# Kernel optimization log

Measured on AMD Instinct MI355X. Metric: run time of the kernel, lower is better.

The kernel has to match this reference:

```python
import jax, jax.numpy as jnp
import numpy as np

B, MAX_NPUS, MEM_SIZE = 16, 1024, 4096
IN_SIZE, REG_SIZE, MEM_DIM = 512, 256, 128
GRU_IN = IN_SIZE + MEM_DIM
MMU_OUT = MEM_DIM * 5 + 4  # 644


def setup_inputs() -> dict:
    key = jax.random.key(0)
    ks = jax.random.split(key, 12)
    s = 0.02
    return {
        "input_vector": jax.random.normal(ks[0], (B, IN_SIZE), jnp.float32),
        "registers": jax.random.normal(ks[1], (B, MAX_NPUS, REG_SIZE), jnp.float32),
        "memory_context": jax.random.normal(ks[2], (B, MEM_SIZE, MEM_DIM), jnp.float32),
        "W_ih": jax.random.normal(ks[3], (3 * REG_SIZE, GRU_IN), jnp.float32) * s,
        "b_ih": jax.random.normal(ks[4], (3 * REG_SIZE,), jnp.float32) * s,
        "W_hh": jax.random.normal(ks[5], (3 * REG_SIZE, REG_SIZE), jnp.float32) * s,
        "b_hh": jax.random.normal(ks[6], (3 * REG_SIZE,), jnp.float32) * s,
        "W_mmu": jax.random.normal(ks[7], (MMU_OUT, REG_SIZE), jnp.float32) * s,
        "b_mmu": jax.random.normal(ks[8], (MMU_OUT,), jnp.float32) * s,
        "W_out": jax.random.normal(ks[9], (IN_SIZE, REG_SIZE), jnp.float32) * s,
        "b_out": jax.random.normal(ks[10], (IN_SIZE,), jnp.float32) * s,
        "active_npus": MAX_NPUS,
    }


def reference(input_vector, registers, memory_context, W_ih, b_ih, W_hh, b_hh,
              W_mmu, b_mmu, W_out, b_out, active_npus):
    md, rs = MEM_DIM, REG_SIZE
    curr = registers[:, :active_npus, :]                      # [B,N,rs]
    mmu = jnp.einsum('bnr,or->bno', curr, W_mmu) + b_mmu      # [B,N,5*md+4]
    query = mmu[..., :md]
    w_key = mmu[..., md:2 * md]
    w_val = mmu[..., 2 * md:3 * md]
    w_gate = jax.nn.sigmoid(mmu[..., 3 * md:3 * md + 1])
    ssd_key = mmu[..., 3 * md + 1:4 * md + 1]
    ssd_val = mmu[..., 4 * md + 1:5 * md + 1]
    ssd_gate = jax.nn.softmax(mmu[..., 5 * md + 1:5 * md + 4], axis=-1)
    # attention read over shared memory
    scores = jnp.einsum('bnd,bmd->bnm', query, memory_context) / jnp.sqrt(jnp.float32(md))
    attn = jax.nn.softmax(scores, axis=-1)                    # [B,N,M]
    read_data = jnp.einsum('bnm,bmd->bnd', attn, memory_context)
    # GRU cell (torch GRUCell semantics, gate order r,z,n)
    inp = jnp.broadcast_to(input_vector[:, None, :], (curr.shape[0], active_npus, input_vector.shape[-1]))
    x = jnp.concatenate([inp, read_data], axis=-1)            # [B,N,in+md]
    gi = jnp.einsum('bni,oi->bno', x, W_ih) + b_ih            # [B,N,3*rs]
    gh = jnp.einsum('bnr,or->bno', curr, W_hh) + b_hh
    gi_r, gi_z, gi_n = gi[..., :rs], gi[..., rs:2 * rs], gi[..., 2 * rs:]
    gh_r, gh_z, gh_n = gh[..., :rs], gh[..., rs:2 * rs], gh[..., 2 * rs:]
    r = jax.nn.sigmoid(gi_r + gh_r)
    z = jax.nn.sigmoid(gi_z + gh_z)
    n = jnp.tanh(gi_n + r * gh_n)
    new_regs = (1.0 - z) * n + z * curr                       # [B,N,rs]
    output_active = jnp.einsum('bnr,or->bno', new_regs, W_out) + b_out
    return (output_active, new_regs, w_key, w_val, w_gate, ssd_key, ssd_val, ssd_gate)
```

## Files before the change

kernel.cpp:

```cpp
#include <hip/hip_runtime.h>
#include <hip/hip_bf16.h>
#include <math.h>

#define B_      16
#define NPUS    1024
#define MEMS    4096
#define INS     512
#define RS      256
#define MD      128
#define GRUIN   640
#define MMUO    644
#define NROWS   (B_*NPUS)

#define O_OUT   0u
#define O_REGS  8388608u
#define O_WKEY  12582912u
#define O_WVAL  14680064u
#define O_WGATE 16777216u
#define O_SSDK  16793600u
#define O_SSDV  18890752u
#define O_SSDG  20987904u

typedef __attribute__((ext_vector_type(8))) short bf16x8;
typedef __attribute__((ext_vector_type(4))) float f32x4;
typedef __attribute__((ext_vector_type(4))) unsigned short u16x4;

__device__ __forceinline__ float sigf(float x){ return 1.f/(1.f+__expf(-x)); }
__device__ __forceinline__ unsigned short bfu(float x){
    __hip_bfloat16 h = __float2bfloat16(x);
    return __builtin_bit_cast(unsigned short, h);
}
__device__ __forceinline__ float b2f(unsigned short u){
    unsigned v = ((unsigned)u) << 16;
    return __builtin_bit_cast(float, v);
}
__device__ __forceinline__ void gload16(const void* g, void* s)
{
    __builtin_amdgcn_global_load_lds(
        (const __attribute__((address_space(1))) void*)g,
        (__attribute__((address_space(3))) void*)s, 16, 0, 0);
}

__global__ __launch_bounds__(256) void k_cvt(const float* __restrict__ src,
                                             unsigned short* __restrict__ dst, int n4)
{
    int i = blockIdx.x*256 + threadIdx.x;
    if (i >= n4) return;
    float4 v = ((const float4*)src)[i];
    u16x4 o = { bfu(v.x), bfu(v.y), bfu(v.z), bfu(v.w) };
    ((u16x4*)dst)[i] = o;
}

__global__ __launch_bounds__(256) void k_cvt5(const float* __restrict__ s0, unsigned short* __restrict__ d0,
                                              const float* __restrict__ s1, unsigned short* __restrict__ d1,
                                              const float* __restrict__ s2, unsigned short* __restrict__ d2,
                                              const float* __restrict__ s3, unsigned short* __restrict__ d3,
                                              const float* __restrict__ s4, unsigned short* __restrict__ d4)
{
    int gi = blockIdx.x*256 + threadIdx.x;
    const float* s; unsigned short* d; int idx;
    if      (gi < 41216)  { s = s0; d = d0; idx = gi; }
    else if (gi < 164096) { s = s1; d = d1; idx = gi - 41216; }
    else if (gi < 213248) { s = s2; d = d2; idx = gi - 164096; }
    else if (gi < 246016) { s = s3; d = d3; idx = gi - 213248; }
    else                  { s = s4; d = d4; idx = gi - 246016; }
    float4 v = ((const float4*)s)[idx];
    u16x4 o = { bfu(v.x), bfu(v.y), bfu(v.z), bfu(v.w) };
    ((u16x4*)d)[idx] = o;
}

__global__ __launch_bounds__(256) void k_gi(const float* __restrict__ inp,
                                            const float* __restrict__ Wih,
                                            float* __restrict__ gi0)
{
    __shared__ float xs[INS];
    const int b = blockIdx.x, seg = blockIdx.y;
    const int t = threadIdx.x;
    for (int i = t; i < INS; i += 256) xs[i] = inp[(size_t)b*INS + i];
    __syncthreads();
    const int o = seg*256 + t;
    const float* wrow = Wih + (size_t)o*GRUIN;
    float a0 = 0.f, a1 = 0.f, a2 = 0.f, a3 = 0.f;
    for (int k = 0; k < INS; k += 4) {
        float4 wv = *(const float4*)(wrow + k);
        a0 += xs[k]*wv.x; a1 += xs[k+1]*wv.y; a2 += xs[k+2]*wv.z; a3 += xs[k+3]*wv.w;
    }
    gi0[(size_t)b*768 + o] = (a0 + a1) + (a2 + a3);
}

__global__ __launch_bounds__(256) void k_conv(const float* __restrict__ mem,
                                              __hip_bfloat16* __restrict__ memB,
                                              __hip_bfloat16* __restrict__ memT)
{
    __shared__ float Ms[32][129];
    const int t = threadIdx.x;
    const int b = blockIdx.x >> 7;
    const int m0 = (blockIdx.x & 127) << 5;
    const float* src = mem + ((size_t)b*MEMS + m0)*MD;
    for (int idx = t; idx < 32*128; idx += 256) {
        int m = idx >> 7, d = idx & 127;
        float v = src[(size_t)m*MD + d];
        Ms[m][d] = v;
        memB[((size_t)b*MEMS + m0 + m)*MD + d] = __float2bfloat16(v);
    }
    __syncthreads();
    for (int idx = t; idx < 128*32; idx += 256) {
        int d = idx >> 5, m = idx & 31;
        memT[((size_t)b*MD + d)*MEMS + m0 + m] = __float2bfloat16(Ms[m][d]);
    }
}

__global__ __launch_bounds__(256, 4) void k_mmu(const __hip_bfloat16* __restrict__ Ab,
                                                const __hip_bfloat16* __restrict__ Wb,
                                                const float* __restrict__ bias,
                                                float* __restrict__ out,
                                                __hip_bfloat16* __restrict__ qbf)
{
    __shared__ __hip_bfloat16 At[2][64][32];
    __shared__ __hip_bfloat16 Bt[2][128][32];
    const int t = threadIdx.x, w = t >> 6, l = t & 63;
    const int lg = l >> 4, ll = l & 15;
    const int m0 = blockIdx.x*64;
    const int n0 = blockIdx.y*128;
    f32x4 acc[8];
    #pragma unroll
    for (int c = 0; c < 8; c++) acc[c] = (f32x4){0,0,0,0};

    const char* aSrc;
    {
        int row = t >> 2, cc = t & 3;
        int gc = cc ^ ((row >> 1) & 3);
        aSrc = (const char*)((const short*)Ab + (size_t)(m0+row)*RS) + gc*16;
    }
    const char* bSrc[2];
    #pragma unroll
    for (int j = 0; j < 2; j++) {
        int ci = w*128 + j*64 + l;
        int row = ci >> 2, cc = ci & 3;
        int gc = cc ^ ((row >> 1) & 3);
        bSrc[j] = (const char*)((const short*)Wb + (size_t)(n0+row)*RS) + gc*16;
    }

    auto stage = [&](int buf, int it) {
        int off = it*64;
        char* abase = (char*)(&At[buf][0][0]) + (size_t)(w << 6)*16;
        gload16(aSrc + off, abase);
        #pragma unroll
        for (int j = 0; j < 2; j++) {
            char* bbase = (char*)(&Bt[buf][0][0]) + (size_t)(w*128 + j*64)*16;
            gload16(bSrc[j] + off, bbase);
        }
    };

    stage(0, 0);
    asm volatile("s_waitcnt vmcnt(0)" ::: "memory");
    __syncthreads();
    int cur = 0;
    const int arow = (w << 4) + ll;
    const int aswz = ((lg ^ ((arow >> 1) & 3)) << 4);
    for (int it = 0; it < 8; ++it) {
        if (it + 1 < 8) stage(cur ^ 1, it + 1);
        const char* ab = (const char*)(&At[cur][0][0]);
        const char* bb = (const char*)(&Bt[cur][0][0]);
        bf16x8 af = *(const bf16x8*)(ab + arow*64 + aswz);
        #pragma unroll
        for (int c = 0; c < 8; c++) {
            int r0 = c*16 + ll;
            int sw = ((lg ^ ((r0 >> 1) & 3)) << 4);
            bf16x8 bf = *(const bf16x8*)(bb + (size_t)r0*64 + sw);
            acc[c] = __builtin_amdgcn_mfma_f32_16x16x32_bf16(af, bf, acc[c], 0, 0, 0);
        }
        asm volatile("s_waitcnt vmcnt(0)" ::: "memory");
        __syncthreads();
        cur ^= 1;
    }
    const int wm0 = m0 + (w << 4);
    #pragma unroll
    for (int c = 0; c < 8; c++) {
        int o = n0 + c*16 + ll;
        if (o > 640) continue;
        float bv = bias[o];
        #pragma unroll
        for (int r = 0; r < 4; r++) {
            int row = wm0 + lg*4 + r;
            float v = acc[c][r] + bv;
            if      (o < MD)        qbf[(size_t)row*MD + o] = __float2bfloat16(v * 0.08838834764831845f);
            else if (o < 2*MD)      out[O_WKEY + (size_t)row*MD + (o -   MD)] = v;
            else if (o < 3*MD)      out[O_WVAL + (size_t)row*MD + (o - 2*MD)] = v;
            else if (o == 3*MD)     out[O_WGATE + row] = sigf(v);
            else if (o < 4*MD + 1)  out[O_SSDK + (size_t)row*MD + (o - (3*MD+1))] = v;
            else                    out[O_SSDV + (size_t)row*MD + (o - (4*MD+1))] = v;
        }
    }
    if (n0 == 640) {
        #pragma unroll
        for (int r = 0; r < 4; r++) {
            int o = n0 + ll;
            float vr = acc[0][r] + ((o < MMUO) ? bias[o] : 0.f);
            float va = __shfl(vr, lg*16 + 1);
            float vb = __shfl(vr, lg*16 + 2);
            float vc = __shfl(vr, lg*16 + 3);
            float mm = fmaxf(va, fmaxf(vb, vc));
            float ea = __expf(va-mm), eb = __expf(vb-mm), ec = __expf(vc-mm);
            float inv = 1.f/(ea+eb+ec);
            int row = wm0 + lg*4 + r;
            if (ll == 1) out[O_SSDG + (size_t)row*3 + 0] = ea*inv;
            if (ll == 2) out[O_SSDG + (size_t)row*3 + 1] = eb*inv;
            if (ll == 3) out[O_SSDG + (size_t)row*3 + 2] = ec*inv;
        }
    }
}

__global__ __launch_bounds__(256, 4) void k_attn(const __hip_bfloat16* __restrict__ qb,
                                                 const __hip_bfloat16* __restrict__ memB,
                                                 const __hip_bfloat16* __restrict__ memT,
                                                 unsigned short* __restrict__ Opart,
                                                 float* __restrict__ MLpart)
{
    __shared__ __hip_bfloat16 Kt[2][32][128];
    __shared__ __hip_bfloat16 Vt[2][128][32];
    __shared__ __hip_bfloat16 Pl[4][16][40];
    const int t = threadIdx.x, w = t >> 6, l = t & 63;
    const int lg = l >> 4, ll = l & 15;
    const int bid = blockIdx.x;
    const int xcd = bid & 7, rest = bid >> 3;
    const int b = xcd + ((rest >> 6) << 3);
    const int sub = rest & 63;
    const int qblk = sub >> 2, kh = sub & 3;
    const int qrow0 = (b << 10) + (qblk << 6) + (w << 4);
    const int k_beg = kh << 10;
    const float THR = 4.0f;

    const short* Q = (const short*)qb;
    bf16x8 qf[4];
    #pragma unroll
    for (int ks = 0; ks < 4; ks++)
        qf[ks] = *(const bf16x8*)(Q + (size_t)(qrow0 + ll)*MD + ks*32 + lg*8);

    f32x4 O[8];
    #pragma unroll
    for (int dt = 0; dt < 8; dt++) O[dt] = (f32x4){0.f,0.f,0.f,0.f};
    float m_run[4], lsum[4];
    #pragma unroll
    for (int r = 0; r < 4; r++) { m_run[r] = -INFINITY; lsum[r] = 0.f; }

    const char* MbB = (const char*)memB + (size_t)b*MEMS*MD*2;
    const char* MtB = (const char*)memT + (size_t)b*MD*MEMS*2;

    auto stage = [&](int buf, int it) {
        const int k0 = k_beg + it*32;
        char* kbase = (char*)(&Kt[buf][0][0]);
        char* vbase = (char*)(&Vt[buf][0][0]);
        #pragma unroll
        for (int j = 0; j < 2; j++) {
            int ci = (w << 7) + (j << 6) + l;
            int krow = ci >> 4, cc = ci & 15;
            int gc = cc ^ (krow & 7);
            gload16(MbB + (size_t)(k0 + krow)*256 + gc*16,
                    kbase + (size_t)((w << 7) + (j << 6))*16);
        }
        #pragma unroll
        for (int j = 0; j < 2; j++) {
            int ci = (w << 7) + (j << 6) + l;
            int drow = ci >> 2, cc = ci & 3;
            int gc = cc ^ ((drow >> 1) & 3);
            gload16(MtB + (size_t)drow*(MEMS*2) + (size_t)k0*2 + gc*16,
                    vbase + (size_t)((w << 7) + (j << 6))*16);
        }
    };

    stage(0, 0);
    asm volatile("s_waitcnt vmcnt(0)" ::: "memory");
    asm volatile("s_barrier" ::: "memory");
    int cur = 0;
    const int NIT = 1024/32;
    const int vsw = ((lg ^ ((ll >> 1) & 3)) << 4);
    for (int it = 0; it < NIT; ++it) {
        if (it + 1 < NIT) {
            stage(cur ^ 1, it + 1);
            asm volatile("s_waitcnt vmcnt(4)" ::: "memory");
        } else {
            asm volatile("s_waitcnt vmcnt(0)" ::: "memory");
        }
        asm volatile("s_barrier" ::: "memory");
        const char* kbase = (const char*)(&Kt[cur][0][0]);
        const char* vbase = (const char*)(&Vt[cur][0][0]);
        f32x4 s0 = (f32x4){0,0,0,0}, s1 = (f32x4){0,0,0,0};
        #pragma unroll
        for (int ks = 0; ks < 4; ks++) {
            int c0 = ks*4 + lg;
            int sw = (c0 ^ (ll & 7)) << 4;
            bf16x8 kf0 = *(const bf16x8*)(kbase + (size_t)ll*256 + sw);
            bf16x8 kf1 = *(const bf16x8*)(kbase + (size_t)(16 + ll)*256 + sw);
            s0 = __builtin_amdgcn_mfma_f32_16x16x32_bf16(qf[ks], kf0, s0, 0, 0, 0);
            s1 = __builtin_amdgcn_mfma_f32_16x16x32_bf16(qf[ks], kf1, s1, 0, 0, 0);
        }
        bool need = false;
        #pragma unroll
        for (int r = 0; r < 4; r++) {
            need |= (s0[r] > m_run[r] + THR);
            need |= (s1[r] > m_run[r] + THR);
        }
        if (__any(need)) {
            #pragma unroll
            for (int r = 0; r < 4; r++) {
                float v = fmaxf(s0[r], s1[r]);
                v = fmaxf(v, __shfl_xor(v, 1));
                v = fmaxf(v, __shfl_xor(v, 2));
                v = fmaxf(v, __shfl_xor(v, 4));
                v = fmaxf(v, __shfl_xor(v, 8));
                float mnew = fmaxf(m_run[r], v);
                float alpha = __expf(m_run[r] - mnew);
                m_run[r] = mnew;
                lsum[r] *= alpha;
                #pragma unroll
                for (int dt = 0; dt < 8; dt++) O[dt][r] *= alpha;
            }
        }
        #pragma unroll
        for (int r = 0; r < 4; r++) {
            float p0 = __expf(s0[r] - m_run[r]);
            float p1 = __expf(s1[r] - m_run[r]);
            Pl[w][lg*4 + r][ll]      = __float2bfloat16(p0);
            Pl[w][lg*4 + r][16 + ll] = __float2bfloat16(p1);
            lsum[r] += p0 + p1;
        }
        __builtin_amdgcn_wave_barrier();
        bf16x8 pa = *(const bf16x8*)(&Pl[w][ll][lg*8]);
        __builtin_amdgcn_wave_barrier();
        #pragma unroll
        for (int dt = 0; dt < 8; dt++) {
            bf16x8 vf = *(const bf16x8*)(vbase + (size_t)(dt*16 + ll)*64 + vsw);
            O[dt] = __builtin_amdgcn_mfma_f32_16x16x32_bf16(pa, vf, O[dt], 0, 0, 0);
        }
        asm volatile("s_barrier" ::: "memory");
        cur ^= 1;
    }
    #pragma unroll
    for (int r = 0; r < 4; r++) {
        float s = lsum[r];
        s += __shfl_xor(s, 1);
        s += __shfl_xor(s, 2);
        s += __shfl_xor(s, 4);
        s += __shfl_xor(s, 8);
        lsum[r] = s;
    }
    #pragma unroll
    for (int dt = 0; dt < 8; dt++)
        #pragma unroll
        for (int r = 0; r < 4; r++) {
            int row = qrow0 + lg*4 + r;
            Opart[((size_t)row*4 + kh)*128 + dt*16 + ll] = bfu(O[dt][r]);
        }
    if (ll == 0) {
        #pragma unroll
        for (int r = 0; r < 4; r++) {
            int row = qrow0 + lg*4 + r;
            MLpart[((size_t)row*4 + kh)*2 + 0] = m_run[r];
            MLpart[((size_t)row*4 + kh)*2 + 1] = lsum[r];
        }
    }
}

__global__ __launch_bounds__(256) void k_comb(const unsigned short* __restrict__ Opart,
                                              const float* __restrict__ MLpart,
                                              __hip_bfloat16* __restrict__ rdb)
{
    const int t = threadIdx.x;
    const int row = blockIdx.x*64 + (t >> 2);
    const int c0 = (t & 3) * 32;
    float m[4], lv[4], a[4];
    float M = -INFINITY;
    #pragma unroll
    for (int i = 0; i < 4; i++) {
        m[i]  = MLpart[((size_t)row*4 + i)*2 + 0];
        lv[i] = MLpart[((size_t)row*4 + i)*2 + 1];
        M = fmaxf(M, m[i]);
    }
    float L = 0.f;
    #pragma unroll
    for (int i = 0; i < 4; i++) { a[i] = __expf(m[i] - M); L += a[i]*lv[i]; }
    float invL = 1.f / L;
    #pragma unroll
    for (int i = 0; i < 4; i++) a[i] *= invL;
    unsigned short* dst = (unsigned short*)rdb + (size_t)row*128 + c0;
    #pragma unroll
    for (int j = 0; j < 8; j++) {
        float acc0=0.f, acc1=0.f, acc2=0.f, acc3=0.f;
        #pragma unroll
        for (int i = 0; i < 4; i++) {
            u16x4 x = ((const u16x4*)(Opart + ((size_t)row*4 + i)*128 + c0))[j];
            acc0 += a[i]*b2f(x[0]); acc1 += a[i]*b2f(x[1]);
            acc2 += a[i]*b2f(x[2]); acc3 += a[i]*b2f(x[3]);
        }
        u16x4 o = { bfu(acc0), bfu(acc1), bfu(acc2), bfu(acc3) };
        ((u16x4*)dst)[j] = o;
    }
}

__global__ __launch_bounds__(256, 4) void k_gru(const float* __restrict__ gi0,
                                                const __hip_bfloat16* __restrict__ rdb,
                                                const __hip_bfloat16* __restrict__ regsb,
                                                const float* __restrict__ regs,
                                                const __hip_bfloat16* __restrict__ Wihb,
                                                const float* __restrict__ bih,
                                                const __hip_bfloat16* __restrict__ Whhb,
                                                const float* __restrict__ bhh,
                                                float* __restrict__ newregs,
                                                __hip_bfloat16* __restrict__ nregsb)
{
    __shared__ __hip_bfloat16 At[2][64][32];
    __shared__ __hip_bfloat16 Bt[2][192][32];
    const int t = threadIdx.x, w = t >> 6, l = t & 63;
    const int lg = l >> 4, ll = l & 15;
    const int m0 = blockIdx.x*64;
    const int n0 = blockIdx.y*64;
    const int batch = blockIdx.x >> 4;
    const short* Rd = (const short*)rdb;
    const short* Hb = (const short*)regsb;
    const short* Wi = (const short*)Wihb;
    const short* Wh = (const short*)Whhb;

    f32x4 aR[4], aZ[4], aNi[4], aNh[4];
    #pragma unroll
    for (int c = 0; c < 4; c++) {
        int o = n0 + c*16 + ll;
        float gR = gi0[(size_t)batch*768 + o];
        float gZ = gi0[(size_t)batch*768 + 256 + o];
        float gN = gi0[(size_t)batch*768 + 512 + o];
        aR[c]  = (f32x4){gR,gR,gR,gR};
        aZ[c]  = (f32x4){gZ,gZ,gZ,gZ};
        aNi[c] = (f32x4){gN,gN,gN,gN};
        aNh[c] = (f32x4){0,0,0,0};
    }

    const int aci = (w << 6) + l;
    const int arow_s = aci >> 2, acc_s = aci & 3;
    const int agc = acc_s ^ ((arow_s >> 1) & 3);
    const char* aSrcA = (const char*)(Rd + (size_t)(m0+arow_s)*MD) + agc*16;
    const char* aSrcB = (const char*)(Hb + (size_t)(m0+arow_s)*RS) + agc*16;
    const char* bSrcA0; const char* bSrcA1; const char* bSrcA2;
    const char* bSrcB0; const char* bSrcB1; const char* bSrcB2;
    {
        int ci, row, cc, gc, g, col;
        ci = w*192 + 0*64 + l; row = ci >> 2; cc = ci & 3; gc = cc ^ ((row >> 1) & 3);
        g = row >> 6; col = row & 63;
        bSrcA0 = (const char*)(Wi + (size_t)(g*RS + n0 + col)*GRUIN + INS) + gc*16;
        bSrcB0 = (const char*)(Wh + (size_t)(g*RS + n0 + col)*RS) + gc*16;
        ci = w*192 + 1*64 + l; row = ci >> 2; cc = ci & 3; gc = cc ^ ((row >> 1) & 3);
        g = row >> 6; col = row & 63;
        bSrcA1 = (const char*)(Wi + (size_t)(g*RS + n0 + col)*GRUIN + INS) + gc*16;
        bSrcB1 = (const char*)(Wh + (size_t)(g*RS + n0 + col)*RS) + gc*16;
        ci = w*192 + 2*64 + l; row = ci >> 2; cc = ci & 3; gc = cc ^ ((row >> 1) & 3);
        g = row >> 6; col = row & 63;
        bSrcA2 = (const char*)(Wi + (size_t)(g*RS + n0 + col)*GRUIN + INS) + gc*16;
        bSrcB2 = (const char*)(Wh + (size_t)(g*RS + n0 + col)*RS) + gc*16;
    }

    const int NITA = 4, NIT = 12;
    auto stage = [&](int buf, int it) {
        char* abase = (char*)(&At[buf][0][0]) + (size_t)(w << 6)*16;
        char* bbase = (char*)(&Bt[buf][0][0]) + (size_t)(w*192)*16;
        const char *as, *b0, *b1, *b2;
        if (it < NITA) {
            int off = it*64;
            as = aSrcA + off; b0 = bSrcA0 + off; b1 = bSrcA1 + off; b2 = bSrcA2 + off;
        } else {
            int off = (it - NITA)*64;
            as = aSrcB + off; b0 = bSrcB0 + off; b1 = bSrcB1 + off; b2 = bSrcB2 + off;
        }
        gload16(as, abase);
        gload16(b0, bbase);
        gload16(b1, bbase + 64*16);
        gload16(b2, bbase + 128*16);
    };

    stage(0, 0);
    asm volatile("s_waitcnt vmcnt(0)" ::: "memory");
    __syncthreads();
    int cur = 0;
    const int arow = (w << 4) + ll;
    const int aswz = ((lg ^ ((arow >> 1) & 3)) << 4);
    for (int it = 0; it < NIT; ++it) {
        if (it + 1 < NIT) stage(cur ^ 1, it + 1);
        const char* ab = (const char*)(&At[cur][0][0]);
        const char* bb = (const char*)(&Bt[cur][0][0]);
        bf16x8 af = *(const bf16x8*)(ab + arow*64 + aswz);
        if (it < NITA) {
            #pragma unroll
            for (int c = 0; c < 4; c++) {
                int r0 = c*16 + ll;
                int sw = ((lg ^ ((r0 >> 1) & 3)) << 4);
                bf16x8 bR = *(const bf16x8*)(bb + (size_t)r0*64 + sw);
                bf16x8 bZ = *(const bf16x8*)(bb + (size_t)(r0 + 64)*64 + sw);
                bf16x8 bN = *(const bf16x8*)(bb + (size_t)(r0 + 128)*64 + sw);
                aR[c]  = __builtin_amdgcn_mfma_f32_16x16x32_bf16(af, bR, aR[c],  0, 0, 0);
                aZ[c]  = __builtin_amdgcn_mfma_f32_16x16x32_bf16(af, bZ, aZ[c],  0, 0, 0);
                aNi[c] = __builtin_amdgcn_mfma_f32_16x16x32_bf16(af, bN, aNi[c], 0, 0, 0);
            }
        } else {
            #pragma unroll
            for (int c = 0; c < 4; c++) {
                int r0 = c*16 + ll;
                int sw = ((lg ^ ((r0 >> 1) & 3)) << 4);
                bf16x8 bR = *(const bf16x8*)(bb + (size_t)r0*64 + sw);
                bf16x8 bZ = *(const bf16x8*)(bb + (size_t)(r0 + 64)*64 + sw);
                bf16x8 bN = *(const bf16x8*)(bb + (size_t)(r0 + 128)*64 + sw);
                aR[c]  = __builtin_amdgcn_mfma_f32_16x16x32_bf16(af, bR, aR[c],  0, 0, 0);
                aZ[c]  = __builtin_amdgcn_mfma_f32_16x16x32_bf16(af, bZ, aZ[c],  0, 0, 0);
                aNh[c] = __builtin_amdgcn_mfma_f32_16x16x32_bf16(af, bN, aNh[c], 0, 0, 0);
            }
        }
        asm volatile("s_waitcnt vmcnt(0)" ::: "memory");
        __syncthreads();
        cur ^= 1;
    }
    const int wm0 = m0 + (w << 4);
    #pragma unroll
    for (int c = 0; c < 4; c++) {
        int o = n0 + c*16 + ll;
        float bR = bih[o]        + bhh[o];
        float bZ = bih[o +   RS] + bhh[o +   RS];
        float bNi = bih[o + 2*RS];
        float bNh = bhh[o + 2*RS];
        #pragma unroll
        for (int r = 0; r < 4; r++) {
            int row = wm0 + lg*4 + r;
            float rr = sigf(aR[c][r] + bR);
            float zz = sigf(aZ[c][r] + bZ);
            float nn = tanhf(aNi[c][r] + bNi + rr*(aNh[c][r] + bNh));
            float cv = regs[(size_t)row*RS + o];
            float nv = (1.f - zz)*nn + zz*cv;
            newregs[(size_t)row*RS + o] = nv;
            nregsb[(size_t)row*RS + o] = __float2bfloat16(nv);
        }
    }
}

__global__ __launch_bounds__(256, 4) void k_out(const __hip_bfloat16* __restrict__ Ab,
                                                const __hip_bfloat16* __restrict__ Wb,
                                                const float* __restrict__ bias,
                                                float* __restrict__ out0)
{
    __shared__ __hip_bfloat16 At[2][64][32];
    __shared__ __hip_bfloat16 Bt[2][128][32];
    const int t = threadIdx.x, w = t >> 6, l = t & 63;
    const int lg = l >> 4, ll = l & 15;
    const int m0 = blockIdx.x*64;
    const int n0 = blockIdx.y*128;
    f32x4 acc[8];
    #pragma unroll
    for (int c = 0; c < 8; c++) acc[c] = (f32x4){0,0,0,0};

    const char* aSrc;
    {
        int row = t >> 2, cc = t & 3;
        int gc = cc ^ ((row >> 1) & 3);
        aSrc = (const char*)((const short*)Ab + (size_t)(m0+row)*RS) + gc*16;
    }
    const char* bSrc[2];
    #pragma unroll
    for (int j = 0; j < 2; j++) {
        int ci = w*128 + j*64 + l;
        int row = ci >> 2, cc = ci & 3;
        int gc = cc ^ ((row >> 1) & 3);
        bSrc[j] = (const char*)((const short*)Wb + (size_t)(n0+row)*RS) + gc*16;
    }

    auto stage = [&](int buf, int it) {
        int off = it*64;
        char* abase = (char*)(&At[buf][0][0]) + (size_t)(w << 6)*16;
        gload16(aSrc + off, abase);
        #pragma unroll
        for (int j = 0; j < 2; j++) {
            char* bbase = (char*)(&Bt[buf][0][0]) + (size_t)(w*128 + j*64)*16;
            gload16(bSrc[j] + off, bbase);
        }
    };

    stage(0, 0);
    asm volatile("s_waitcnt vmcnt(0)" ::: "memory");
    __syncthreads();
    int cur = 0;
    const int arow = (w << 4) + ll;
    const int aswz = ((lg ^ ((arow >> 1) & 3)) << 4);
    for (int it = 0; it < 8; ++it) {
        if (it + 1 < 8) stage(cur ^ 1, it + 1);
        const char* ab = (const char*)(&At[cur][0][0]);
        const char* bb = (const char*)(&Bt[cur][0][0]);
        bf16x8 af = *(const bf16x8*)(ab + arow*64 + aswz);
        #pragma unroll
        for (int c = 0; c < 8; c++) {
            int r0 = c*16 + ll;
            int sw = ((lg ^ ((r0 >> 1) & 3)) << 4);
            bf16x8 bf = *(const bf16x8*)(bb + (size_t)r0*64 + sw);
            acc[c] = __builtin_amdgcn_mfma_f32_16x16x32_bf16(af, bf, acc[c], 0, 0, 0);
        }
        asm volatile("s_waitcnt vmcnt(0)" ::: "memory");
        __syncthreads();
        cur ^= 1;
    }
    const int wm0 = m0 + (w << 4);
    #pragma unroll
    for (int c = 0; c < 8; c++) {
        int o = n0 + c*16 + ll;
        float bv = bias[o];
        #pragma unroll
        for (int r = 0; r < 4; r++) {
            int row = wm0 + lg*4 + r;
            out0[(size_t)row*INS + o] = acc[c][r] + bv;
        }
    }
}

extern "C" void kernel_launch(void* const* d_in, const int* in_sizes, int n_in,
                              void* d_out, int out_size, void* d_ws, size_t ws_size,
                              hipStream_t stream)
{
    const float* inp  = (const float*)d_in[0];
    const float* regs = (const float*)d_in[1];
    const float* mem  = (const float*)d_in[2];
    const float* Wih  = (const float*)d_in[3];
    const float* bih  = (const float*)d_in[4];
    const float* Whh  = (const float*)d_in[5];
    const float* bhh  = (const float*)d_in[6];
    const float* Wmmu = (const float*)d_in[7];
    const float* bmmu = (const float*)d_in[8];
    const float* Wout = (const float*)d_in[9];
    const float* bout = (const float*)d_in[10];
    float* out = (float*)d_out;

    char* ws = (char*)d_ws;
    __hip_bfloat16* qbf    = (__hip_bfloat16*)(ws);
    __hip_bfloat16* rdb    = (__hip_bfloat16*)(ws + ((size_t)4<<20));
    __hip_bfloat16* memB   = (__hip_bfloat16*)(ws + ((size_t)8<<20));
    __hip_bfloat16* memT   = (__hip_bfloat16*)(ws + ((size_t)24<<20));
    __hip_bfloat16* regsb  = (__hip_bfloat16*)(ws + ((size_t)40<<20));
    __hip_bfloat16* nregsb = (__hip_bfloat16*)(ws + ((size_t)48<<20));
    __hip_bfloat16* Wmmub  = (__hip_bfloat16*)(ws + ((size_t)56<<20));
    __hip_bfloat16* Wihb   = (__hip_bfloat16*)(ws + ((size_t)56<<20) + ( 1<<20));
    __hip_bfloat16* Whhb   = (__hip_bfloat16*)(ws + ((size_t)56<<20) + ( 2<<20));
    __hip_bfloat16* Woutb  = (__hip_bfloat16*)(ws + ((size_t)56<<20) + ( 3<<20));
    __hip_bfloat16* inpb   = (__hip_bfloat16*)(ws + ((size_t)56<<20) + ( 4<<20));
    float*          MLpart = (float*)(ws + ((size_t)61<<20));
    float*          gi0    = (float*)(ws + ((size_t)61<<20) + (1<<19));
    unsigned short* Opart  = (unsigned short*)(out + O_OUT);

    dim3 ggi(B_, 3);
    k_gi<<<ggi, 256, 0, stream>>>(inp, Wih, gi0);
    k_cvt5<<<969, 256, 0, stream>>>(Wmmu, (unsigned short*)Wmmub,
                                    Wih,  (unsigned short*)Wihb,
                                    Whh,  (unsigned short*)Whhb,
                                    Wout, (unsigned short*)Woutb,
                                    inp,  (unsigned short*)inpb);
    k_cvt<<<(4194304/4 + 255)/256, 256, 0, stream>>>(regs, (unsigned short*)regsb, 4194304/4);
    k_conv<<<B_*128, 256, 0, stream>>>(mem, memB, memT);

    dim3 g1(NROWS/64, 6);
    k_mmu<<<g1, 256, 0, stream>>>(regsb, Wmmub, bmmu, out, qbf);
    k_attn<<<1024, 256, 0, stream>>>(qbf, memB, memT, Opart, MLpart);
    k_comb<<<NROWS/64, 256, 0, stream>>>(Opart, MLpart, rdb);
    dim3 g3(NROWS/64, 4);
    k_gru<<<g3, 256, 0, stream>>>(gi0, rdb, regsb, regs, Wihb, bih, Whhb, bhh,
                                  out + O_REGS, nregsb);
    dim3 g4(NROWS/64, 4);
    k_out<<<g4, 256, 0, stream>>>(nregsb, Woutb, bout, out);
}
```

Before: 158.0 us.

## Process two query tiles per wave in attention and fold gi GEMV into convert kernel

The attention kernel now has each wave handle 32 query rows (two 16-row MFMA tiles), so each K/V tile staged in shared memory is reused twice and V fragments are loaded into registers once per iteration. The grid halves to 512 blocks and the occupancy hint drops to 2 blocks per CU to allow for the higher register use. Separately, the small gi GEMV kernel is merged into the weight-conversion kernel as extra blocks, saving one launch. The trade-off is fewer concurrent waves for latency hiding and more register pressure in exchange for halved LDS/K-V traffic per query.

```diff
diff --git a/kernel.cpp b/kernel.cpp
--- a/kernel.cpp
+++ b/kernel.cpp
@@ -51,12 +51,30 @@
     ((u16x4*)dst)[i] = o;
 }
 
-__global__ __launch_bounds__(256) void k_cvt5(const float* __restrict__ s0, unsigned short* __restrict__ d0,
-                                              const float* __restrict__ s1, unsigned short* __restrict__ d1,
-                                              const float* __restrict__ s2, unsigned short* __restrict__ d2,
-                                              const float* __restrict__ s3, unsigned short* __restrict__ d3,
-                                              const float* __restrict__ s4, unsigned short* __restrict__ d4)
-{
+__global__ __launch_bounds__(256) void k_cvt5g(const float* __restrict__ s0, unsigned short* __restrict__ d0,
+                                               const float* __restrict__ s1, unsigned short* __restrict__ d1,
+                                               const float* __restrict__ s2, unsigned short* __restrict__ d2,
+                                               const float* __restrict__ s3, unsigned short* __restrict__ d3,
+                                               const float* __restrict__ s4, unsigned short* __restrict__ d4,
+                                               float* __restrict__ gi0)
+{
+    __shared__ float xs[INS];
+    if (blockIdx.x >= 969) {
+        const int gb = blockIdx.x - 969;
+        const int b = gb / 3, seg = gb % 3;
+        const int t = threadIdx.x;
+        for (int i = t; i < INS; i += 256) xs[i] = s4[(size_t)b*INS + i];
+        __syncthreads();
+        const int o = seg*256 + t;
+        const float* wrow = s1 + (size_t)o*GRUIN;
+        float a0 = 0.f, a1 = 0.f, a2 = 0.f, a3 = 0.f;
+        for (int k = 0; k < INS; k += 4) {
+            float4 wv = *(const float4*)(wrow + k);
+            a0 += xs[k]*wv.x; a1 += xs[k+1]*wv.y; a2 += xs[k+2]*wv.z; a3 += xs[k+3]*wv.w;
+        }
+        gi0[(size_t)b*768 + o] = (a0 + a1) + (a2 + a3);
+        return;
+    }
     int gi = blockIdx.x*256 + threadIdx.x;
     const float* s; unsigned short* d; int idx;
     if      (gi < 41216)  { s = s0; d = d0; idx = gi; }
@@ -67,25 +85,6 @@
     float4 v = ((const float4*)s)[idx];
     u16x4 o = { bfu(v.x), bfu(v.y), bfu(v.z), bfu(v.w) };
     ((u16x4*)d)[idx] = o;
-}
-
-__global__ __launch_bounds__(256) void k_gi(const float* __restrict__ inp,
-                                            const float* __restrict__ Wih,
-                                            float* __restrict__ gi0)
-{
-    __shared__ float xs[INS];
-    const int b = blockIdx.x, seg = blockIdx.y;
-    const int t = threadIdx.x;
-    for (int i = t; i < INS; i += 256) xs[i] = inp[(size_t)b*INS + i];
-    __syncthreads();
-    const int o = seg*256 + t;
-    const float* wrow = Wih + (size_t)o*GRUIN;
-    float a0 = 0.f, a1 = 0.f, a2 = 0.f, a3 = 0.f;
-    for (int k = 0; k < INS; k += 4) {
-        float4 wv = *(const float4*)(wrow + k);
-        a0 += xs[k]*wv.x; a1 += xs[k+1]*wv.y; a2 += xs[k+2]*wv.z; a3 += xs[k+3]*wv.w;
-    }
-    gi0[(size_t)b*768 + o] = (a0 + a1) + (a2 + a3);
 }
 
 __global__ __launch_bounds__(256) void k_conv(const float* __restrict__ mem,
@@ -211,7 +210,7 @@
     }
 }
 
-__global__ __launch_bounds__(256, 4) void k_attn(const __hip_bfloat16* __restrict__ qb,
+__global__ __launch_bounds__(256, 2) void k_attn(const __hip_bfloat16* __restrict__ qb,
                                                  const __hip_bfloat16* __restrict__ memB,
                                                  const __hip_bfloat16* __restrict__ memT,
                                                  unsigned short* __restrict__ Opart,
@@ -224,25 +223,31 @@
     const int lg = l >> 4, ll = l & 15;
     const int bid = blockIdx.x;
     const int xcd = bid & 7, rest = bid >> 3;
-    const int b = xcd + ((rest >> 6) << 3);
-    const int sub = rest & 63;
+    const int b = xcd + ((rest >> 5) << 3);
+    const int sub = rest & 31;
     const int qblk = sub >> 2, kh = sub & 3;
-    const int qrow0 = (b << 10) + (qblk << 6) + (w << 4);
+    const int qrow0 = (b << 10) + (qblk << 7) + (w << 5);
     const int k_beg = kh << 10;
     const float THR = 4.0f;
 
     const short* Q = (const short*)qb;
-    bf16x8 qf[4];
-    #pragma unroll
-    for (int ks = 0; ks < 4; ks++)
-        qf[ks] = *(const bf16x8*)(Q + (size_t)(qrow0 + ll)*MD + ks*32 + lg*8);
-
-    f32x4 O[8];
-    #pragma unroll
-    for (int dt = 0; dt < 8; dt++) O[dt] = (f32x4){0.f,0.f,0.f,0.f};
-    float m_run[4], lsum[4];
-    #pragma unroll
-    for (int r = 0; r < 4; r++) { m_run[r] = -INFINITY; lsum[r] = 0.f; }
+    bf16x8 qf[2][4];
+    #pragma unroll
+    for (int qs = 0; qs < 2; qs++)
+        #pragma unroll
+        for (int ks = 0; ks < 4; ks++)
+            qf[qs][ks] = *(const bf16x8*)(Q + (size_t)(qrow0 + qs*16 + ll)*MD + ks*32 + lg*8);
+
+    f32x4 O[2][8];
+    #pragma unroll
+    for (int qs = 0; qs < 2; qs++)
+        #pragma unroll
+        for (int dt = 0; dt < 8; dt++) O[qs][dt] = (f32x4){0.f,0.f,0.f,0.f};
+    float m_run[2][4], lsum[2][4];
+    #pragma unroll
+    for (int qs = 0; qs < 2; qs++)
+        #pragma unroll
+        for (int r = 0; r < 4; r++) { m_run[qs][r] = -INFINITY; lsum[qs][r] = 0.f; }
 
     const char* MbB = (const char*)memB + (size_t)b*MEMS*MD*2;
     const char* MtB = (const char*)memT + (size_t)b*MD*MEMS*2;
@@ -285,80 +290,99 @@
         asm volatile("s_barrier" ::: "memory");
         const char* kbase = (const char*)(&Kt[cur][0][0]);
         const char* vbase = (const char*)(&Vt[cur][0][0]);
-        f32x4 s0 = (f32x4){0,0,0,0}, s1 = (f32x4){0,0,0,0};
+        bf16x8 vf[8];
+        #pragma unroll
+        for (int dt = 0; dt < 8; dt++)
+            vf[dt] = *(const bf16x8*)(vbase + (size_t)(dt*16 + ll)*64 + vsw);
+        f32x4 s[2][2];
+        s[0][0]=(f32x4){0,0,0,0}; s[0][1]=(f32x4){0,0,0,0};
+        s[1][0]=(f32x4){0,0,0,0}; s[1][1]=(f32x4){0,0,0,0};
         #pragma unroll
         for (int ks = 0; ks < 4; ks++) {
             int c0 = ks*4 + lg;
             int sw = (c0 ^ (ll & 7)) << 4;
             bf16x8 kf0 = *(const bf16x8*)(kbase + (size_t)ll*256 + sw);
             bf16x8 kf1 = *(const bf16x8*)(kbase + (size_t)(16 + ll)*256 + sw);
-            s0 = __builtin_amdgcn_mfma_f32_16x16x32_bf16(qf[ks], kf0, s0, 0, 0, 0);
-            s1 = __builtin_amdgcn_mfma_f32_16x16x32_bf16(qf[ks], kf1, s1, 0, 0, 0);
+            s[0][0] = __builtin_amdgcn_mfma_f32_16x16x32_bf16(qf[0][ks], kf0, s[0][0], 0, 0, 0);
+            s[1][0] = __builtin_amdgcn_mfma_f32_16x16x32_bf16(qf[1][ks], kf0, s[1][0], 0, 0, 0);
+            s[0][1] = __builtin_amdgcn_mfma_f32_16x16x32_bf16(qf[0][ks], kf1, s[0][1], 0, 0, 0);
+            s[1][1] = __builtin_amdgcn_mfma_f32_16x16x32_bf16(qf[1][ks], kf1, s[1][1], 0, 0, 0);
         }
         bool need = false;
         #pragma unroll
-        for (int r = 0; r < 4; r++) {
-            need |= (s0[r] > m_run[r] + THR);
-            need |= (s1[r] > m_run[r] + THR);
-        }
+        for (int qs = 0; qs < 2; qs++)
+            #pragma unroll
+            for (int r = 0; r < 4; r++) {
+                need |= (s[qs][0][r] > m_run[qs][r] + THR);
+                need |= (s[qs][1][r] > m_run[qs][r] + THR);
+            }
         if (__any(need)) {
             #pragma unroll
+            for (int qs = 0; qs < 2; qs++)
+                #pragma unroll
+                for (int r = 0; r < 4; r++) {
+                    float v = fmaxf(s[qs][0][r], s[qs][1][r]);
+                    v = fmaxf(v, __shfl_xor(v, 1));
+                    v = fmaxf(v, __shfl_xor(v, 2));
+                    v = fmaxf(v, __shfl_xor(v, 4));
+                    v = fmaxf(v, __shfl_xor(v, 8));
+                    float mnew = fmaxf(m_run[qs][r], v);
+                    float alpha = __expf(m_run[qs][r] - mnew);
+                    m_run[qs][r] = mnew;
+                    lsum[qs][r] *= alpha;
+                    #pragma unroll
+                    for (int dt = 0; dt < 8; dt++) O[qs][dt][r] *= alpha;
+                }
+        }
+        #pragma unroll
+        for (int qs = 0; qs < 2; qs++) {
+            #pragma unroll
             for (int r = 0; r < 4; r++) {
-                float v = fmaxf(s0[r], s1[r]);
-                v = fmaxf(v, __shfl_xor(v, 1));
-                v = fmaxf(v, __shfl_xor(v, 2));
-                v = fmaxf(v, __shfl_xor(v, 4));
-                v = fmaxf(v, __shfl_xor(v, 8));
-                float mnew = fmaxf(m_run[r], v);
-                float alpha = __expf(m_run[r] - mnew);
-                m_run[r] = mnew;
-                lsum[r] *= alpha;
-                #pragma unroll
-                for (int dt = 0; dt < 8; dt++) O[dt][r] *= alpha;
+                float p0 = __expf(s[qs][0][r] - m_run[qs][r]);
+                float p1 = __expf(s[qs][1][r] - m_run[qs][r]);
+                Pl[w][lg*4 + r][ll]      = __float2bfloat16(p0);
+                Pl[w][lg*4 + r][16 + ll] = __float2bfloat16(p1);
+                lsum[qs][r] += p0 + p1;
             }
-        }
-        #pragma unroll
-        for (int r = 0; r < 4; r++) {
-            float p0 = __expf(s0[r] - m_run[r]);
-            float p1 = __expf(s1[r] - m_run[r]);
-            Pl[w][lg*4 + r][ll]      = __float2bfloat16(p0);
-            Pl[w][lg*4 + r][16 + ll] = __float2bfloat16(p1);
-            lsum[r] += p0 + p1;
-        }
-        __builtin_amdgcn_wave_barrier();
-        bf16x8 pa = *(const bf16x8*)(&Pl[w][ll][lg*8]);
-        __builtin_amdgcn_wave_barrier();
-        #pragma unroll
-        for (int dt = 0; dt < 8; dt++) {
-            bf16x8 vf = *(const bf16x8*)(vbase + (size_t)(dt*16 + ll)*64 + vsw);
-            O[dt] = __builtin_amdgcn_mfma_f32_16x16x32_bf16(pa, vf, O[dt], 0, 0, 0);
+            __builtin_amdgcn_wave_barrier();
+            bf16x8 pa = *(const bf16x8*)(&Pl[w][ll][lg*8]);
+            __builtin_amdgcn_wave_barrier();
+            #pragma unroll
+            for (int dt = 0; dt < 8; dt++)
+                O[qs][dt] = __builtin_amdgcn_mfma_f32_16x16x32_bf16(pa, vf[dt], O[qs][dt], 0, 0, 0);
         }
         asm volatile("s_barrier" ::: "memory");
         cur ^= 1;
     }
     #pragma unroll
-    for (int r = 0; r < 4; r++) {
-        float s = lsum[r];
-        s += __shfl_xor(s, 1);
-        s += __shfl_xor(s, 2);
-        s += __shfl_xor(s, 4);
-        s += __shfl_xor(s, 8);
-        lsum[r] = s;
-    }
-    #pragma unroll
-    for (int dt = 0; dt < 8; dt++)
+    for (int qs = 0; qs < 2; qs++)
         #pragma unroll
         for (int r = 0; r < 4; r++) {
-            int row = qrow0 + lg*4 + r;
-            Opart[((size_t)row*4 + kh)*128 + dt*16 + ll] = bfu(O[dt][r]);
-        }
+            float s2 = lsum[qs][r];
+            s2 += __shfl_xor(s2, 1);
+            s2 += __shfl_xor(s2, 2);
+            s2 += __shfl_xor(s2, 4);
+            s2 += __shfl_xor(s2, 8);
+            lsum[qs][r] = s2;
+        }
+    #pragma unroll
+    for (int qs = 0; qs < 2; qs++)
+        #pragma unroll
+        for (int dt = 0; dt < 8; dt++)
+            #pragma unroll
+            for (int r = 0; r < 4; r++) {
+                int row = qrow0 + qs*16 + lg*4 + r;
+                Opart[((size_t)row*4 + kh)*128 + dt*16 + ll] = bfu(O[qs][dt][r]);
+            }
     if (ll == 0) {
         #pragma unroll
-        for (int r = 0; r < 4; r++) {
-            int row = qrow0 + lg*4 + r;
-            MLpart[((size_t)row*4 + kh)*2 + 0] = m_run[r];
-            MLpart[((size_t)row*4 + kh)*2 + 1] = lsum[r];
-        }
+        for (int qs = 0; qs < 2; qs++)
+            #pragma unroll
+            for (int r = 0; r < 4; r++) {
+                int row = qrow0 + qs*16 + lg*4 + r;
+                MLpart[((size_t)row*4 + kh)*2 + 0] = m_run[qs][r];
+                MLpart[((size_t)row*4 + kh)*2 + 1] = lsum[qs][r];
+            }
     }
 }
 
@@ -646,19 +670,17 @@
     float*          gi0    = (float*)(ws + ((size_t)61<<20) + (1<<19));
     unsigned short* Opart  = (unsigned short*)(out + O_OUT);
 
-    dim3 ggi(B_, 3);
-    k_gi<<<ggi, 256, 0, stream>>>(inp, Wih, gi0);
-    k_cvt5<<<969, 256, 0, stream>>>(Wmmu, (unsigned short*)Wmmub,
-                                    Wih,  (unsigned short*)Wihb,
-                                    Whh,  (unsigned short*)Whhb,
-                                    Wout, (unsigned short*)Woutb,
-                                    inp,  (unsigned short*)inpb);
+    k_cvt5g<<<1017, 256, 0, stream>>>(Wmmu, (unsigned short*)Wmmub,
+                                      Wih,  (unsigned short*)Wihb,
+                                      Whh,  (unsigned short*)Whhb,
+                                      Wout, (unsigned short*)Woutb,
+                                      inp,  (unsigned short*)inpb, gi0);
     k_cvt<<<(4194304/4 + 255)/256, 256, 0, stream>>>(regs, (unsigned short*)regsb, 4194304/4);
     k_conv<<<B_*128, 256, 0, stream>>>(mem, memB, memT);
 
     dim3 g1(NROWS/64, 6);
     k_mmu<<<g1, 256, 0, stream>>>(regsb, Wmmub, bmmu, out, qbf);
-    k_attn<<<1024, 256, 0, stream>>>(qbf, memB, memT, Opart, MLpart);
+    k_attn<<<512, 256, 0, stream>>>(qbf, memB, memT, Opart, MLpart);
     k_comb<<<NROWS/64, 256, 0, stream>>>(Opart, MLpart, rdb);
     dim3 g3(NROWS/64, 4);
     k_gru<<<g3, 256, 0, stream>>>(gi0, rdb, regsb, regs, Wihb, bih, Whhb, bhh,
```

Result: no change. 155.4 us (-1.6%).
